# Performance work log

Measured on AMD Instinct MI355X. Metric: run time of the kernel, lower is better.

The kernel has to match this reference:

```python
import jax, jax.numpy as jnp
import numpy as np


def _euclidean_cdist(x, q):
    # torch.cdist with p=2: pairwise L2 distances, shape [B, Q]
    x2 = jnp.sum(x * x, axis=-1, keepdims=True)          # [B, 1]
    q2 = jnp.sum(q * q, axis=-1)[None, :]                # [1, Q]
    d2 = x2 + q2 - 2.0 * (x @ q.T)                        # [B, Q]
    return jnp.sqrt(jnp.maximum(d2, 0.0))


def setup_inputs() -> dict:
    key = jax.random.key(0)
    k1, k2 = jax.random.split(key)
    x = jax.random.normal(k1, (1024, 256), dtype=jnp.float32)
    queue = jax.random.normal(k2, (32768, 256), dtype=jnp.float32)
    return {"x": x, "queue": queue}


def reference(x, queue):
    # Queue update: concat then keep the newest max_size rows (queue assumed full)
    max_size = queue.shape[0]
    q = jnp.concatenate([queue, x], axis=0)[-max_size:]   # [Q, F]
    # Distance matrix + top-2 nearest (topk of negated distances)
    d = _euclidean_cdist(x, q)                            # [B, Q]
    _, idx = jax.lax.top_k(-d, 2)                         # [B, 2]
    # Second-nearest neighbor (first is the point itself, dist 0)
    return q[idx[:, 1]]                                   # [B, F]
```

## Files before the change

### kernel.cpp

```cpp
#include <hip/hip_runtime.h>
#include <stdint.h>

#define B_ROWS 1024
#define FEAT   256
#define QSZ    32768
#define SHIFT  1024
#define QX     (QSZ - B_ROWS)
#define NQB    256
#define NXB    8
#define MARGIN 20.0f

typedef float v4f __attribute__((ext_vector_type(4)));
typedef int   v4i __attribute__((ext_vector_type(4)));
typedef int   v8i __attribute__((ext_vector_type(8)));

__device__ __forceinline__ uint32_t key_flip(uint32_t u) {
    return u ^ ((uint32_t)((int32_t)u >> 31) | 0x80000000u);
}
__device__ __forceinline__ float key_m(uint32_t k) {
    uint32_t u = k & 0xFFFF8000u;
    u = (u & 0x80000000u) ? (u ^ 0x80000000u) : ~u;
    return __uint_as_float(u);
}
__device__ __forceinline__ void k2_insert(uint32_t& k1, uint32_t& k2, uint32_t key) {
    uint32_t hi = max(k1, key); k1 = min(k1, key); k2 = min(k2, hi);
}
__device__ __forceinline__ uint2 k2_merge(uint2 a, uint2 b) {
    uint32_t hi = max(a.x, b.x);
    uint2 r; r.x = min(a.x, b.x); r.y = min(min(a.y, b.y), hi);
    return r;
}

struct Top2 { float m1; int j1; float m2; int j2; };
__device__ __forceinline__ bool better(float ma, int ja, float mb, int jb) {
    return (ma < mb) || (ma == mb && ja < jb);
}
__device__ __forceinline__ void t2_insert(Top2& t, float m, int j) {
    if (better(m, j, t.m1, t.j1)) { t.m2 = t.m1; t.j2 = t.j1; t.m1 = m; t.j1 = j; }
    else if (better(m, j, t.m2, t.j2)) { t.m2 = m; t.j2 = j; }
}

__device__ __forceinline__ const float* q_row_ptr(int j, const float* x, const float* queue) {
    return (j < QX) ? (queue + (size_t)(j + SHIFT) * FEAT) : (x + (size_t)(j - QX) * FEAT);
}

__device__ __forceinline__ void lds_load16(const void* g, void* l) {
    __builtin_amdgcn_global_load_lds(
        (const __attribute__((address_space(1))) uint32_t*)g,
        (__attribute__((address_space(3))) uint32_t*)l, 16, 0, 0);
}

__global__ __launch_bounds__(256) void convert_kernel(const float* __restrict__ x,
                                                      const float* __restrict__ queue,
                                                      uint32_t* __restrict__ q_f8,
                                                      float* __restrict__ q2) {
    int wave = threadIdx.x >> 6, lane = threadIdx.x & 63;
    int j = blockIdx.x * 4 + wave;
    const float4* row = (const float4*)q_row_ptr(j, x, queue);
    float4 v = row[lane];
    float s = v.x * v.x + v.y * v.y + v.z * v.z + v.w * v.w;
#pragma unroll
    for (int off = 32; off; off >>= 1) s += __shfl_xor(s, off, 64);
    if (lane == 0) q2[j] = s;
    uint32_t u = __builtin_amdgcn_cvt_pk_fp8_f32(v.x, v.y, 0, false);
    u = __builtin_amdgcn_cvt_pk_fp8_f32(v.z, v.w, u, true);
    q_f8[(size_t)j * 64 + lane] = u;
}

__global__ __launch_bounds__(256, 3) void nn_mfma(const uint8_t* __restrict__ q_f8,
                                                  const float* __restrict__ q2,
                                                  uint2* __restrict__ partials) {
    __shared__ uint8_t As[128 * 128];
    __shared__ uint8_t Bs[128 * 128];
    __shared__ float sq2[128];
    __shared__ uint2 scr[128][2];

    const int t    = threadIdx.x;
    const int w    = t >> 6, lane = t & 63;
    const int wm   = w >> 1, wn = w & 1;
    const int quad = lane >> 4, l16 = lane & 15;
    const int gy   = blockIdx.x;
    const int gx   = blockIdx.y;

    const uint8_t* x_f8 = q_f8 + (size_t)QX * FEAT;

    if (t < 128) sq2[t] = q2[gy * 128 + t];

    v4f acc[4][4];
#pragma unroll
    for (int a = 0; a < 4; ++a)
#pragma unroll
        for (int b = 0; b < 4; ++b) acc[a][b] = (v4f)0.0f;

    const int srow = lane >> 3;
    const int sg   = (lane & 7) ^ srow;
    const int gsw  = l16 & 7;
    const int g0   = (2 * quad) ^ gsw;
    const int g1   = (2 * quad + 1) ^ gsw;

    for (int c = 0; c < 2; ++c) {
        __syncthreads();
#pragma unroll
        for (int kk = 0; kk < 4; ++kk) {
            int row = w * 32 + kk * 8 + srow;
            const uint8_t* ga = q_f8 + (size_t)(gy * 128 + row) * FEAT + c * 128 + sg * 16;
            const uint8_t* gb = x_f8 + (size_t)(gx * 128 + row) * FEAT + c * 128 + sg * 16;
            lds_load16(ga, &As[(w * 32 + kk * 8) * 128]);
            lds_load16(gb, &Bs[(w * 32 + kk * 8) * 128]);
        }
        __syncthreads();
        const uint8_t* arow = As + (wm * 64 + l16) * 128;
        const uint8_t* brow = Bs + (wn * 64 + l16) * 128;
        v8i fa[4], fb[4];
#pragma unroll
        for (int tm = 0; tm < 4; ++tm) {
            v4i lo = *(const v4i*)(arow + tm * 2048 + g0 * 16);
            v4i hi = *(const v4i*)(arow + tm * 2048 + g1 * 16);
            fa[tm][0] = lo[0]; fa[tm][1] = lo[1]; fa[tm][2] = lo[2]; fa[tm][3] = lo[3];
            fa[tm][4] = hi[0]; fa[tm][5] = hi[1]; fa[tm][6] = hi[2]; fa[tm][7] = hi[3];
        }
#pragma unroll
        for (int tn = 0; tn < 4; ++tn) {
            v4i lo = *(const v4i*)(brow + tn * 2048 + g0 * 16);
            v4i hi = *(const v4i*)(brow + tn * 2048 + g1 * 16);
            fb[tn][0] = lo[0]; fb[tn][1] = lo[1]; fb[tn][2] = lo[2]; fb[tn][3] = lo[3];
            fb[tn][4] = hi[0]; fb[tn][5] = hi[1]; fb[tn][6] = hi[2]; fb[tn][7] = hi[3];
        }
#pragma unroll
        for (int tm = 0; tm < 4; ++tm)
#pragma unroll
            for (int tn = 0; tn < 4; ++tn)
                acc[tm][tn] = __builtin_amdgcn_mfma_scale_f32_16x16x128_f8f6f4(
                    fa[tm], fb[tn], acc[tm][tn],
                    0, 0,
                    0, 0x7F7F7F7F,
                    0, 0x7F7F7F7F);
    }

    float q2r[4][4];
#pragma unroll
    for (int tm = 0; tm < 4; ++tm) {
        v4f qq = *(const v4f*)&sq2[wm * 64 + tm * 16 + quad * 4];
#pragma unroll
        for (int r = 0; r < 4; ++r) q2r[tm][r] = qq[r];
    }
    const int jbase = gy * 128 + wm * 64 + quad * 4;

    uint2 best[4];
#pragma unroll
    for (int tn = 0; tn < 4; ++tn) {
        uint32_t k1 = 0xFFFFFFFFu, k2 = 0xFFFFFFFFu;
#pragma unroll
        for (int tm = 0; tm < 4; ++tm)
#pragma unroll
            for (int r = 0; r < 4; ++r) {
                float m = fmaf(-2.0f, acc[tm][tn][r], q2r[tm][r]);
                uint32_t u = key_flip(__float_as_uint(m));
                uint32_t key = (u & 0xFFFF8000u) | (uint32_t)(jbase + tm * 16 + r);
                k2_insert(k1, k2, key);
            }
#pragma unroll
        for (int mask = 16; mask <= 32; mask <<= 1) {
            uint32_t o1 = __shfl_xor(k1, mask, 64);
            uint32_t o2 = __shfl_xor(k2, mask, 64);
            uint32_t hi = max(k1, o1);
            k1 = min(k1, o1);
            k2 = min(min(k2, o2), hi);
        }
        best[tn] = make_uint2(k1, k2);
    }
    if (quad == 0) {
#pragma unroll
        for (int tn = 0; tn < 4; ++tn) scr[wn * 64 + tn * 16 + l16][wm] = best[tn];
    }
    __syncthreads();
    if (t < 128) {
        uint2 r = k2_merge(scr[t][0], scr[t][1]);
        partials[(size_t)(gx * 128 + t) * NQB + gy] = r;
    }
}

__global__ __launch_bounds__(64) void nn_finalize(const float* __restrict__ x,
                                                  const float* __restrict__ queue,
                                                  const float* __restrict__ q2,
                                                  const uint2* __restrict__ partials,
                                                  float* __restrict__ out) {
    __shared__ int list[64];
    __shared__ int s_cnt;

    const int i = blockIdx.x, lane = threadIdx.x;
    if (lane == 0) s_cnt = 0;

    const uint2* p = partials + (size_t)i * NQB;
    uint2 mine[4];
#pragma unroll
    for (int u = 0; u < 4; ++u) mine[u] = p[lane + 64 * u];
    uint2 a = k2_merge(k2_merge(mine[0], mine[1]), k2_merge(mine[2], mine[3]));
#pragma unroll
    for (int mask = 1; mask <= 32; mask <<= 1) {
        uint2 o;
        o.x = __shfl_xor(a.x, mask, 64);
        o.y = __shfl_xor(a.y, mask, 64);
        a = k2_merge(a, o);
    }
    float cutf = key_m(a.y) + MARGIN;
    uint32_t kcut = key_flip(__float_as_uint(cutf)) | 0x7FFFu;

#pragma unroll
    for (int u = 0; u < 4; ++u) {
        if (mine[u].x <= kcut) list[atomicAdd(&s_cnt, 1) & 63] = (int)(mine[u].x & 0x7FFFu);
        if (mine[u].y <= kcut) list[atomicAdd(&s_cnt, 1) & 63] = (int)(mine[u].y & 0x7FFFu);
    }
    __syncthreads();
    int n = min(s_cnt, 64);

    float4 xv = ((const float4*)(x + (size_t)i * FEAT))[lane];
    Top2 bst;
    bst.m1 = __builtin_inff(); bst.j1 = 0x7FFFFFFF;
    bst.m2 = __builtin_inff(); bst.j2 = 0x7FFFFFFF;
    for (int c = 0; c < n; ++c) {
        int j = list[c];
        float4 qv = ((const float4*)q_row_ptr(j, x, queue))[lane];
        float s = qv.x * xv.x + qv.y * xv.y + qv.z * xv.z + qv.w * xv.w;
#pragma unroll
        for (int off = 32; off; off >>= 1) s += __shfl_xor(s, off, 64);
        float m = q2[j] - 2.0f * s;
        t2_insert(bst, m, j);
    }
    int j2 = bst.j2;
    float4 o = ((const float4*)q_row_ptr(j2, x, queue))[lane];
    ((float4*)(out + (size_t)i * FEAT))[lane] = o;
}

extern "C" void kernel_launch(void* const* d_in, const int* in_sizes, int n_in,
                              void* d_out, int out_size, void* d_ws, size_t ws_size,
                              hipStream_t stream) {
    const float* x     = (const float*)d_in[0];
    const float* queue = (const float*)d_in[1];

    uint32_t* q_f8     = (uint32_t*)d_ws;
    float*    q2       = (float*)((char*)d_ws + (8u << 20));
    uint2*    partials = (uint2*)((char*)d_ws + (9u << 20));

    convert_kernel<<<QSZ / 4, 256, 0, stream>>>(x, queue, q_f8, q2);
    nn_mfma<<<dim3(NQB, NXB), 256, 0, stream>>>((const uint8_t*)q_f8, q2, partials);
    nn_finalize<<<B_ROWS, 64, 0, stream>>>(x, queue, q2, partials, (float*)d_out);
}
```

Baseline: 120.2 us.

## Switch distance GEMM from fp8 to bf16 with 256-row tiles and prefetch

The queue copy is converted to bf16 instead of fp8, and the distance GEMM now uses bf16 16x16x32 MFMAs. Each block computes a 256x128 tile split across two A buffers, with a 1D grid remapped for locality. The next K chunk is loaded into LDS right after each compute step, and the rerank margin drops from 20 to 8. This doubles the bytes of the converted copy and the MFMA work per element, traded for higher dot-product precision that allows a smaller margin and so fewer exact reranks in finalize.

After: 115.2 us. 4.1% less time.

```diff
diff --git a/kernel.cpp b/kernel.cpp
--- a/kernel.cpp
+++ b/kernel.cpp
@@ -7,12 +7,10 @@
 #define SHIFT  1024
 #define QX     (QSZ - B_ROWS)
 #define NQB    256
-#define NXB    8
-#define MARGIN 20.0f
+#define MARGIN 8.0f
 
 typedef float v4f __attribute__((ext_vector_type(4)));
-typedef int   v4i __attribute__((ext_vector_type(4)));
-typedef int   v8i __attribute__((ext_vector_type(8)));
+typedef short v8s __attribute__((ext_vector_type(8)));
 
 __device__ __forceinline__ uint32_t key_flip(uint32_t u) {
     return u ^ ((uint32_t)((int32_t)u >> 31) | 0x80000000u);
@@ -44,6 +42,12 @@
     return (j < QX) ? (queue + (size_t)(j + SHIFT) * FEAT) : (x + (size_t)(j - QX) * FEAT);
 }
 
+__device__ __forceinline__ unsigned short f2bf(float f) {
+    uint32_t u = __float_as_uint(f);
+    uint32_t r = u + 0x7FFFu + ((u >> 16) & 1u);
+    return (unsigned short)(r >> 16);
+}
+
 __device__ __forceinline__ void lds_load16(const void* g, void* l) {
     __builtin_amdgcn_global_load_lds(
         (const __attribute__((address_space(1))) uint32_t*)g,
@@ -52,7 +56,7 @@
 
 __global__ __launch_bounds__(256) void convert_kernel(const float* __restrict__ x,
                                                       const float* __restrict__ queue,
-                                                      uint32_t* __restrict__ q_f8,
+                                                      unsigned short* __restrict__ q_bf,
                                                       float* __restrict__ q2) {
     int wave = threadIdx.x >> 6, lane = threadIdx.x & 63;
     int j = blockIdx.x * 4 + wave;
@@ -62,121 +66,134 @@
 #pragma unroll
     for (int off = 32; off; off >>= 1) s += __shfl_xor(s, off, 64);
     if (lane == 0) q2[j] = s;
-    uint32_t u = __builtin_amdgcn_cvt_pk_fp8_f32(v.x, v.y, 0, false);
-    u = __builtin_amdgcn_cvt_pk_fp8_f32(v.z, v.w, u, true);
-    q_f8[(size_t)j * 64 + lane] = u;
-}
-
-__global__ __launch_bounds__(256, 3) void nn_mfma(const uint8_t* __restrict__ q_f8,
+    ushort4 h;
+    h.x = f2bf(v.x); h.y = f2bf(v.y); h.z = f2bf(v.z); h.w = f2bf(v.w);
+    ((ushort4*)q_bf)[(size_t)j * 64 + lane] = h;
+}
+
+__global__ __launch_bounds__(256, 2) void nn_mfma(const unsigned short* __restrict__ q_bf,
                                                   const float* __restrict__ q2,
                                                   uint2* __restrict__ partials) {
-    __shared__ uint8_t As[128 * 128];
-    __shared__ uint8_t Bs[128 * 128];
-    __shared__ float sq2[128];
-    __shared__ uint2 scr[128][2];
+    __shared__ unsigned short As0[128 * 64];
+    __shared__ unsigned short As1[128 * 64];
+    __shared__ unsigned short Bs[128 * 64];
+    __shared__ float sq2[256];
 
     const int t    = threadIdx.x;
     const int w    = t >> 6, lane = t & 63;
     const int wm   = w >> 1, wn = w & 1;
     const int quad = lane >> 4, l16 = lane & 15;
-    const int gy   = blockIdx.x;
-    const int gx   = blockIdx.y;
-
-    const uint8_t* x_f8 = q_f8 + (size_t)QX * FEAT;
-
-    if (t < 128) sq2[t] = q2[gy * 128 + t];
-
-    v4f acc[4][4];
-#pragma unroll
-    for (int a = 0; a < 4; ++a)
-#pragma unroll
-        for (int b = 0; b < 4; ++b) acc[a][b] = (v4f)0.0f;
+
+    const int id  = blockIdx.x;
+    const int sub = id >> 3;
+    const int gx  = sub & 7;
+    const int gyU = (id & 7) * 16 + (sub >> 3);
+
+    const unsigned short* x_bf  = q_bf + (size_t)QX * FEAT;
+    const unsigned short* aBase = q_bf + (size_t)gyU * 256 * FEAT;
+    const unsigned short* bBase = x_bf + (size_t)gx * 128 * FEAT;
+
+    sq2[t] = q2[gyU * 256 + t];
+
+    v4f acc[2][4][4];
+#pragma unroll
+    for (int h = 0; h < 2; ++h)
+#pragma unroll
+        for (int a = 0; a < 4; ++a)
+#pragma unroll
+            for (int b = 0; b < 4; ++b) acc[h][a][b] = (v4f)0.0f;
 
     const int srow = lane >> 3;
     const int sg   = (lane & 7) ^ srow;
-    const int gsw  = l16 & 7;
-    const int g0   = (2 * quad) ^ gsw;
-    const int g1   = (2 * quad + 1) ^ gsw;
-
-    for (int c = 0; c < 2; ++c) {
+
+#pragma unroll
+    for (int kk = 0; kk < 4; ++kk) {
+        int row = w * 32 + kk * 8 + srow;
+        int ldsrow = (w * 32 + kk * 8) * 64;
+        lds_load16(aBase + (size_t)row * FEAT + sg * 8,         &As0[ldsrow]);
+        lds_load16(aBase + (size_t)(row + 128) * FEAT + sg * 8, &As1[ldsrow]);
+        lds_load16(bBase + (size_t)row * FEAT + sg * 8,         &Bs[ldsrow]);
+    }
+
+    for (int c = 0; c < 4; ++c) {
         __syncthreads();
 #pragma unroll
-        for (int kk = 0; kk < 4; ++kk) {
-            int row = w * 32 + kk * 8 + srow;
-            const uint8_t* ga = q_f8 + (size_t)(gy * 128 + row) * FEAT + c * 128 + sg * 16;
-            const uint8_t* gb = x_f8 + (size_t)(gx * 128 + row) * FEAT + c * 128 + sg * 16;
-            lds_load16(ga, &As[(w * 32 + kk * 8) * 128]);
-            lds_load16(gb, &Bs[(w * 32 + kk * 8) * 128]);
+        for (int ks = 0; ks < 2; ++ks) {
+            v8s fa0[4], fa1[4], fb[4];
+            const int goff  = (((ks * 4 + quad) ^ (l16 & 7)) << 4);
+            const int abase = (wm * 64 + l16) * 128 + goff;
+            const int bbase = (wn * 64 + l16) * 128 + goff;
+#pragma unroll
+            for (int tm = 0; tm < 4; ++tm) {
+                fa0[tm] = *(const v8s*)((const char*)As0 + abase + tm * 2048);
+                fa1[tm] = *(const v8s*)((const char*)As1 + abase + tm * 2048);
+            }
+#pragma unroll
+            for (int tn = 0; tn < 4; ++tn)
+                fb[tn] = *(const v8s*)((const char*)Bs + bbase + tn * 2048);
+#pragma unroll
+            for (int tm = 0; tm < 4; ++tm)
+#pragma unroll
+                for (int tn = 0; tn < 4; ++tn) {
+                    acc[0][tm][tn] = __builtin_amdgcn_mfma_f32_16x16x32_bf16(fa0[tm], fb[tn], acc[0][tm][tn], 0, 0, 0);
+                    acc[1][tm][tn] = __builtin_amdgcn_mfma_f32_16x16x32_bf16(fa1[tm], fb[tn], acc[1][tm][tn], 0, 0, 0);
+                }
         }
         __syncthreads();
-        const uint8_t* arow = As + (wm * 64 + l16) * 128;
-        const uint8_t* brow = Bs + (wn * 64 + l16) * 128;
-        v8i fa[4], fb[4];
-#pragma unroll
-        for (int tm = 0; tm < 4; ++tm) {
-            v4i lo = *(const v4i*)(arow + tm * 2048 + g0 * 16);
-            v4i hi = *(const v4i*)(arow + tm * 2048 + g1 * 16);
-            fa[tm][0] = lo[0]; fa[tm][1] = lo[1]; fa[tm][2] = lo[2]; fa[tm][3] = lo[3];
-            fa[tm][4] = hi[0]; fa[tm][5] = hi[1]; fa[tm][6] = hi[2]; fa[tm][7] = hi[3];
-        }
+        if (c < 3) {
+#pragma unroll
+            for (int kk = 0; kk < 4; ++kk) {
+                int row = w * 32 + kk * 8 + srow;
+                int ldsrow = (w * 32 + kk * 8) * 64;
+                lds_load16(aBase + (size_t)row * FEAT + (c + 1) * 64 + sg * 8,         &As0[ldsrow]);
+                lds_load16(aBase + (size_t)(row + 128) * FEAT + (c + 1) * 64 + sg * 8, &As1[ldsrow]);
+                lds_load16(bBase + (size_t)row * FEAT + (c + 1) * 64 + sg * 8,         &Bs[ldsrow]);
+            }
+        }
+    }
+
+    uint2* scr = (uint2*)As0;
+#pragma unroll
+    for (int h = 0; h < 2; ++h) {
+        float q2r[4][4];
+#pragma unroll
+        for (int tm = 0; tm < 4; ++tm)
+#pragma unroll
+            for (int r = 0; r < 4; ++r)
+                q2r[tm][r] = sq2[h * 128 + wm * 64 + tm * 16 + quad * 4 + r];
+        const int jbase = gyU * 256 + h * 128 + wm * 64 + quad * 4;
+
 #pragma unroll
         for (int tn = 0; tn < 4; ++tn) {
-            v4i lo = *(const v4i*)(brow + tn * 2048 + g0 * 16);
-            v4i hi = *(const v4i*)(brow + tn * 2048 + g1 * 16);
-            fb[tn][0] = lo[0]; fb[tn][1] = lo[1]; fb[tn][2] = lo[2]; fb[tn][3] = lo[3];
-            fb[tn][4] = hi[0]; fb[tn][5] = hi[1]; fb[tn][6] = hi[2]; fb[tn][7] = hi[3];
-        }
-#pragma unroll
-        for (int tm = 0; tm < 4; ++tm)
-#pragma unroll
-            for (int tn = 0; tn < 4; ++tn)
-                acc[tm][tn] = __builtin_amdgcn_mfma_scale_f32_16x16x128_f8f6f4(
-                    fa[tm], fb[tn], acc[tm][tn],
-                    0, 0,
-                    0, 0x7F7F7F7F,
-                    0, 0x7F7F7F7F);
-    }
-
-    float q2r[4][4];
-#pragma unroll
-    for (int tm = 0; tm < 4; ++tm) {
-        v4f qq = *(const v4f*)&sq2[wm * 64 + tm * 16 + quad * 4];
-#pragma unroll
-        for (int r = 0; r < 4; ++r) q2r[tm][r] = qq[r];
-    }
-    const int jbase = gy * 128 + wm * 64 + quad * 4;
-
-    uint2 best[4];
-#pragma unroll
-    for (int tn = 0; tn < 4; ++tn) {
-        uint32_t k1 = 0xFFFFFFFFu, k2 = 0xFFFFFFFFu;
-#pragma unroll
-        for (int tm = 0; tm < 4; ++tm)
-#pragma unroll
-            for (int r = 0; r < 4; ++r) {
-                float m = fmaf(-2.0f, acc[tm][tn][r], q2r[tm][r]);
-                uint32_t u = key_flip(__float_as_uint(m));
-                uint32_t key = (u & 0xFFFF8000u) | (uint32_t)(jbase + tm * 16 + r);
-                k2_insert(k1, k2, key);
+            uint32_t k1 = 0xFFFFFFFFu, k2 = 0xFFFFFFFFu;
+#pragma unroll
+            for (int tm = 0; tm < 4; ++tm)
+#pragma unroll
+                for (int r = 0; r < 4; ++r) {
+                    float m = fmaf(-2.0f, acc[h][tm][tn][r], q2r[tm][r]);
+                    uint32_t u = key_flip(__float_as_uint(m));
+                    uint32_t key = (u & 0xFFFF8000u) | (uint32_t)(jbase + tm * 16 + r);
+                    k2_insert(k1, k2, key);
+                }
+#pragma unroll
+            for (int mask = 16; mask <= 32; mask <<= 1) {
+                uint32_t o1 = __shfl_xor(k1, mask, 64);
+                uint32_t o2 = __shfl_xor(k2, mask, 64);
+                uint32_t hi = max(k1, o1);
+                k1 = min(k1, o1);
+                k2 = min(min(k2, o2), hi);
             }
-#pragma unroll
-        for (int mask = 16; mask <= 32; mask <<= 1) {
-            uint32_t o1 = __shfl_xor(k1, mask, 64);
-            uint32_t o2 = __shfl_xor(k2, mask, 64);
-            uint32_t hi = max(k1, o1);
-            k1 = min(k1, o1);
-            k2 = min(min(k2, o2), hi);
-        }
-        best[tn] = make_uint2(k1, k2);
-    }
-    if (quad == 0) {
-#pragma unroll
-        for (int tn = 0; tn < 4; ++tn) scr[wn * 64 + tn * 16 + l16][wm] = best[tn];
+            if (quad == 0)
+                scr[(h * 128 + wn * 64 + tn * 16 + l16) * 2 + wm] = make_uint2(k1, k2);
+        }
     }
     __syncthreads();
     if (t < 128) {
-        uint2 r = k2_merge(scr[t][0], scr[t][1]);
-        partials[(size_t)(gx * 128 + t) * NQB + gy] = r;
+#pragma unroll
+        for (int h = 0; h < 2; ++h) {
+            uint2 r = k2_merge(scr[(h * 128 + t) * 2], scr[(h * 128 + t) * 2 + 1]);
+            partials[(size_t)(gx * 128 + t) * NQB + (gyU * 2 + h)] = r;
+        }
     }
 }
 
@@ -238,11 +255,11 @@
     const float* x     = (const float*)d_in[0];
     const float* queue = (const float*)d_in[1];
 
-    uint32_t* q_f8     = (uint32_t*)d_ws;
-    float*    q2       = (float*)((char*)d_ws + (8u << 20));
-    uint2*    partials = (uint2*)((char*)d_ws + (9u << 20));
-
-    convert_kernel<<<QSZ / 4, 256, 0, stream>>>(x, queue, q_f8, q2);
-    nn_mfma<<<dim3(NQB, NXB), 256, 0, stream>>>((const uint8_t*)q_f8, q2, partials);
+    unsigned short* q_bf     = (unsigned short*)d_ws;
+    float*          q2       = (float*)((char*)d_ws + (16u << 20));
+    uint2*          partials = (uint2*)((char*)d_ws + (17u << 20));
+
+    convert_kernel<<<QSZ / 4, 256, 0, stream>>>(x, queue, q_bf, q2);
+    nn_mfma<<<1024, 256, 0, stream>>>(q_bf, q2, partials);
     nn_finalize<<<B_ROWS, 64, 0, stream>>>(x, queue, q2, partials, (float*)d_out);
 }
```
